# Kernel tuning notes

Hardware: AMD Instinct MI355X
Metric: run time of the kernel (lower is better)

Reference implementation:

```python
import jax, jax.numpy as jnp
import numpy as np

B, C, MID, OUT, T, N = 8, 128, 64, 128, 4, 512


def setup_inputs() -> dict:
    key = jax.random.key(0)
    ks = jax.random.split(key, 5)
    def w(k, o, i, scale):
        return (jax.random.normal(k, (o, i), jnp.float32) * scale)
    return {
        "pc": jax.random.normal(ks[0], (B, C, T, N), jnp.float32),
        "theta_w": w(ks[1], MID, C, 0.05), "theta_b": jnp.zeros((MID,), jnp.float32),
        "phi_w": w(ks[2], MID, C, 0.05), "phi_b": jnp.zeros((MID,), jnp.float32),
        "g_w": w(ks[3], MID, C, 0.05), "g_b": jnp.zeros((MID,), jnp.float32),
        "refine_w": w(ks[4], OUT, MID, 0.05), "refine_b": jnp.zeros((OUT,), jnp.float32),
    }


def reference(pc, theta_w, theta_b, phi_w, phi_b, g_w, g_b, refine_w, refine_b):
    b, c, t, n = pc.shape
    tn = t * n
    # pt_utils.Conv2d with bn=False: 1x1 conv + bias + ReLU
    def proj(wt, bs):
        h = jnp.einsum('oc,bctn->botn', wt, pc) + bs[None, :, None, None]
        return jax.nn.relu(h).reshape(b, -1, tn)  # [B, mid, TN]

    theta = proj(theta_w, theta_b).transpose(0, 2, 1)  # [B, TN, mid]
    phi = proj(phi_w, phi_b)                            # [B, mid, TN]
    g = proj(g_w, g_b).transpose(0, 2, 1)               # [B, TN, mid]

    scores = jnp.einsum('bqm,bmk->bqk', theta, phi)     # [B, TN, TN]
    corr = jax.nn.softmax(scores, axis=1)               # softmax over QUERY axis (dim=1)
    y = jnp.einsum('bqk,bkm->bmq', corr, g)             # bmm then transpose(1,2): [B, mid, TN]

    # pt_utils.Conv1d with bn=False: 1x1 conv + bias + ReLU
    refined = jax.nn.relu(jnp.einsum('om,bmq->boq', refine_w, y) + refine_b[None, :, None])
    # faithful raw reshape (row-major, same as torch) then permute, plus residual
    z = refined.reshape(b, t, n, -1).transpose(0, 3, 1, 2) + pc
    return z
```

## Files before the change

### kernel.cpp

```cpp
#include <hip/hip_runtime.h>


constexpr int NL75_TN  = 2048;
constexpr int NL75_MID = 64;
constexpr int NL75_C   = 128;
constexpr float NL75_L2E = 1.4426950408889634f;

typedef __attribute__((ext_vector_type(8))) short nl75_bf8;
typedef __attribute__((ext_vector_type(4))) float nl75_f4;

__device__ __forceinline__ unsigned short nl75_f2b(float f) {
  unsigned x = __float_as_uint(f);
  return (unsigned short)((x + 0x7fffu + ((x >> 16) & 1u)) >> 16);
}

__device__ __forceinline__ unsigned int nl75_pkbf16(float lo, float hi) {
  unsigned int r;
  asm("v_cvt_pk_bf16_f32 %0, %1, %2" : "=v"(r) : "v"(lo), "v"(hi));
  return r;
}

__device__ __forceinline__ float nl75_exp2(float x) {
  float r;
  asm("v_exp_f32 %0, %1" : "=v"(r) : "v"(x));
  return r;
}

typedef const __attribute__((address_space(1))) unsigned int* nl75_gp;
typedef __attribute__((address_space(3))) unsigned int* nl75_lp;
__device__ __forceinline__ void nl75_gld16(const void* g, void* l) {
  __builtin_amdgcn_global_load_lds((nl75_gp)g, (nl75_lp)l, 16, 0, 0);
}

__device__ __forceinline__ void nl75_stage64(const unsigned short* src,
                                             size_t pitch, unsigned short* lds,
                                             int tid) {
  const int w = tid >> 6, lane = tid & 63;
#pragma unroll
  for (int r = 0; r < 2; r++) {
    const int slot = r * 256 + w * 64 + lane;
    const int row = slot >> 3, x = slot & 7;
    const unsigned short* s =
        src + (size_t)row * pitch + ((x * 8) ^ ((row & 7) << 3));
    nl75_gld16(s, lds + (size_t)(r * 256 + w * 64) * 8);
  }
}

__global__ void NonLocalLayer_75771813036638_kernel() {}

__global__ void nl75_proj(const float* pc, const float* w0, const float* b0,
                          const float* w1, const float* b1, const float* w2,
                          const float* b2, unsigned short* thT,
                          unsigned short* phT, unsigned short* gN, int bOff,
                          int nb) {
  __shared__ float wT[NL75_C][68];
  const int bl = blockIdx.x, pj = blockIdx.y, qt = blockIdx.z;
  const int b = bOff + bl;
  const float* wp = (pj == 0) ? w0 : (pj == 1) ? w1 : w2;
  const float* bp = (pj == 0) ? b0 : (pj == 1) ? b1 : b2;
  const int tid = threadIdx.x;
  for (int i = tid; i < NL75_MID * NL75_C; i += 256)
    wT[i & 127][i >> 7] = wp[i];
  __syncthreads();
  const int qg = tid & 31, mg = tid >> 5;
  const int q = qt * 64 + qg * 2, m0 = mg * 8;
  const float* pcb = pc + (long long)b * NL75_C * NL75_TN + q;
  float acc[8][2];
#pragma unroll
  for (int i = 0; i < 8; i++) acc[i][0] = acc[i][1] = bp[m0 + i];
#pragma unroll 4
  for (int c = 0; c < NL75_C; c++) {
    const float2 p = *(const float2*)&pcb[(size_t)c * NL75_TN];
    float w8[8];
    *(float4*)&w8[0] = *(const float4*)&wT[c][m0];
    *(float4*)&w8[4] = *(const float4*)&wT[c][m0 + 4];
#pragma unroll
    for (int i = 0; i < 8; i++) {
      acc[i][0] = fmaf(w8[i], p.x, acc[i][0]);
      acc[i][1] = fmaf(w8[i], p.y, acc[i][1]);
    }
  }
  if (pj < 2) {
    unsigned int u[8];
#pragma unroll
    for (int i = 0; i < 4; i++) {
      u[i] = nl75_pkbf16(fmaxf(acc[2 * i][0], 0.0f),
                         fmaxf(acc[2 * i + 1][0], 0.0f));
      u[4 + i] = nl75_pkbf16(fmaxf(acc[2 * i][1], 0.0f),
                             fmaxf(acc[2 * i + 1][1], 0.0f));
    }
    unsigned short* dst =
        (pj == 0 ? thT : phT) + ((size_t)bl * NL75_TN + q) * 64 + m0;
    *reinterpret_cast<uint4*>(dst) = *reinterpret_cast<uint4*>(&u[0]);
    *reinterpret_cast<uint4*>(dst + 64) = *reinterpret_cast<uint4*>(&u[4]);
  } else {
    const int kin = q & 63;
    const int np = (kin >> 5) * 32 + (((kin & 15) >> 2) << 3) +
                   (((kin >> 4) & 1) << 2) + (kin & 3);
    const size_t gq = (size_t)(q & ~63) | np;
#pragma unroll
    for (int i = 0; i < 8; i++) {
      ushort2 v;
      v.x = nl75_f2b(fmaxf(acc[i][0], 0.0f));
      v.y = nl75_f2b(fmaxf(acc[i][1], 0.0f));
      *(ushort2*)&gN[((size_t)bl * NL75_MID + m0 + i) * NL75_TN + gq] = v;
    }
  }
}

__global__ void nl75_stats(const unsigned short* thT, const unsigned short* phT,
                           float* Sp, int nb, int qsplit) {
  __shared__ unsigned short thL[2][64 * 64];
  const int bl = blockIdx.x;
  const int kt = blockIdx.y & 15, qs = blockIdx.y >> 4;
  const int tid = threadIdx.x, lane = tid & 63, w = tid >> 6;
  const int l15 = lane & 15, quad = lane >> 4;
  const int k0 = kt * 128;
  const unsigned short* thB = thT + (size_t)bl * NL75_TN * 64;
  const unsigned short* phB = phT + (size_t)bl * NL75_TN * 64;
  const size_t kra = (size_t)(k0 + w * 16 + l15) * 64;
  const size_t krb = (size_t)(k0 + 64 + w * 16 + l15) * 64;
  const nl75_bf8 b0a = *(const nl75_bf8*)&phB[kra + quad * 8];
  const nl75_bf8 b1a = *(const nl75_bf8*)&phB[kra + 32 + quad * 8];
  const nl75_bf8 b0b = *(const nl75_bf8*)&phB[krb + quad * 8];
  const nl75_bf8 b1b = *(const nl75_bf8*)&phB[krb + 32 + quad * 8];
  const int qtN = 32 / qsplit, qtBeg = qs * qtN;
  nl75_stage64(thB + (size_t)(qtBeg * 64) * 64, 64, thL[0], tid);
  __syncthreads();
  float Sa = 0.0f, Sb = 0.0f;
  for (int qt = qtBeg; qt < qtBeg + qtN; qt++) {
    const int cur = (qt - qtBeg) & 1;
    if (qt + 1 < qtBeg + qtN)
      nl75_stage64(thB + (size_t)((qt + 1) * 64) * 64, 64, thL[cur ^ 1], tid);
    __builtin_amdgcn_s_setprio(1);
#pragma unroll
    for (int q16 = 0; q16 < 4; q16++) {
      const int qr = q16 * 16 + l15;
      const int sw = (qr & 7) << 3;
      const nl75_bf8 a0 = *(const nl75_bf8*)&thL[cur][qr * 64 + ((quad * 8) ^ sw)];
      const nl75_bf8 a1 =
          *(const nl75_bf8*)&thL[cur][qr * 64 + ((32 + quad * 8) ^ sw)];
      nl75_f4 ca = {0.0f, 0.0f, 0.0f, 0.0f};
      ca = __builtin_amdgcn_mfma_f32_16x16x32_bf16(a0, b0a, ca, 0, 0, 0);
      ca = __builtin_amdgcn_mfma_f32_16x16x32_bf16(a1, b1a, ca, 0, 0, 0);
      nl75_f4 cb = {0.0f, 0.0f, 0.0f, 0.0f};
      cb = __builtin_amdgcn_mfma_f32_16x16x32_bf16(a0, b0b, cb, 0, 0, 0);
      cb = __builtin_amdgcn_mfma_f32_16x16x32_bf16(a1, b1b, cb, 0, 0, 0);
      Sa += (nl75_exp2(ca[0] * NL75_L2E) + nl75_exp2(ca[1] * NL75_L2E)) +
            (nl75_exp2(ca[2] * NL75_L2E) + nl75_exp2(ca[3] * NL75_L2E));
      Sb += (nl75_exp2(cb[0] * NL75_L2E) + nl75_exp2(cb[1] * NL75_L2E)) +
            (nl75_exp2(cb[2] * NL75_L2E) + nl75_exp2(cb[3] * NL75_L2E));
    }
    __builtin_amdgcn_s_setprio(0);
    __syncthreads();
  }
  Sa += __shfl_xor(Sa, 16);
  Sa += __shfl_xor(Sa, 32);
  Sb += __shfl_xor(Sb, 16);
  Sb += __shfl_xor(Sb, 32);
  if (quad == 0) {
    const long long base = ((long long)(qs * nb + bl)) * NL75_TN + k0;
    Sp[base + w * 16 + l15] = Sa;
    Sp[base + 64 + w * 16 + l15] = Sb;
  }
}

__global__ void nl75_attn(const unsigned short* thT, const unsigned short* phT,
                          const unsigned short* gN, const float* Sp,
                          float* yPart, int nb, int ksplit, int qsplit) {
  __shared__ unsigned short phL[2][64 * 64];
  __shared__ unsigned short gL[2][64 * 64];
  __shared__ float ekL[2048];
  const int wg = blockIdx.x;
  const int bl = wg % nb;
  const int rest = wg / nb;
  const int qt = rest & 15, ks = rest >> 4;
  const int tid = threadIdx.x, lane = tid & 63, w = tid >> 6;
  const int l15 = lane & 15, quad = lane >> 4;
  const int q0 = qt * 128;
  const unsigned short* thB = thT + (size_t)bl * NL75_TN * 64;
  const unsigned short* phB = phT + (size_t)bl * NL75_TN * 64;
  const unsigned short* gB = gN + (size_t)bl * NL75_MID * NL75_TN;
  const int ktN = 32 / ksplit;
  const int ktBeg = ks * ktN, ktEnd = ktBeg + ktN;
  nl75_stage64(phB + (size_t)(ktBeg * 64) * 64, 64, phL[0], tid);
  nl75_stage64(gB + ktBeg * 64, NL75_TN, gL[0], tid);
  nl75_bf8 aq[2][2];
#pragma unroll
  for (int s = 0; s < 2; s++) {
    const size_t qr = (size_t)(q0 + s * 64 + w * 16 + l15) * 64;
    aq[s][0] = *(const nl75_bf8*)&thB[qr + quad * 8];
    aq[s][1] = *(const nl75_bf8*)&thB[qr + 32 + quad * 8];
  }
  const int kRange = ktN * 64;
  for (int kk = tid; kk < kRange; kk += 256) {
    const int k = ktBeg * 64 + kk;
    float S = 0.0f;
    for (int qs = 0; qs < qsplit; qs++)
      S += Sp[((size_t)(qs * nb + bl)) * NL75_TN + k];
    ekL[kk] = __log2f(S);
  }
  nl75_f4 yacc[2][4];
#pragma unroll
  for (int s = 0; s < 2; s++)
#pragma unroll
    for (int i = 0; i < 4; i++) yacc[s][i] = (nl75_f4){0.0f, 0.0f, 0.0f, 0.0f};
  __syncthreads();
  union Frag { nl75_bf8 h; unsigned int u[4]; };
  for (int kt = ktBeg; kt < ktEnd; kt++) {
    const int cur = (kt - ktBeg) & 1;
    if (kt + 1 < ktEnd) {
      nl75_stage64(phB + (size_t)((kt + 1) * 64) * 64, 64, phL[cur ^ 1], tid);
      nl75_stage64(gB + (kt + 1) * 64, NL75_TN, gL[cur ^ 1], tid);
    }
    const int ekBase = (kt - ktBeg) * 64;
    nl75_f4 ek[4];
#pragma unroll
    for (int t = 0; t < 4; t++)
      ek[t] = *(const nl75_f4*)&ekL[ekBase + t * 16 + quad * 4];
    __builtin_amdgcn_s_setprio(1);
    unsigned int pk[2][8];
#pragma unroll
    for (int t = 0; t < 4; t++) {
      const int krr = t * 16 + l15;
      const int sw = (krr & 7) << 3;
      const nl75_bf8 b0 =
          *(const nl75_bf8*)&phL[cur][krr * 64 + ((quad * 8) ^ sw)];
      const nl75_bf8 b1 =
          *(const nl75_bf8*)&phL[cur][krr * 64 + ((32 + quad * 8) ^ sw)];
#pragma unroll
      for (int s = 0; s < 2; s++) {
        nl75_f4 c = {0.0f, 0.0f, 0.0f, 0.0f};
        c = __builtin_amdgcn_mfma_f32_16x16x32_bf16(b0, aq[s][0], c, 0, 0, 0);
        c = __builtin_amdgcn_mfma_f32_16x16x32_bf16(b1, aq[s][1], c, 0, 0, 0);
        pk[s][t * 2 + 0] =
            nl75_pkbf16(nl75_exp2(fmaf(c[0], NL75_L2E, -ek[t][0])),
                        nl75_exp2(fmaf(c[1], NL75_L2E, -ek[t][1])));
        pk[s][t * 2 + 1] =
            nl75_pkbf16(nl75_exp2(fmaf(c[2], NL75_L2E, -ek[t][2])),
                        nl75_exp2(fmaf(c[3], NL75_L2E, -ek[t][3])));
      }
    }
#pragma unroll
    for (int mtile = 0; mtile < 4; mtile++) {
      const int m = mtile * 16 + l15;
      const int sw = (m & 7) << 3;
      const unsigned short* row = &gL[cur][m * 64];
      Frag bg0, bg1;
      bg0.h = *(const nl75_bf8*)&row[(quad * 8) ^ sw];
      bg1.h = *(const nl75_bf8*)&row[(32 + quad * 8) ^ sw];
#pragma unroll
      for (int s = 0; s < 2; s++) {
        Frag a0, a1;
        a0.u[0] = pk[s][0]; a0.u[1] = pk[s][1];
        a0.u[2] = pk[s][2]; a0.u[3] = pk[s][3];
        a1.u[0] = pk[s][4]; a1.u[1] = pk[s][5];
        a1.u[2] = pk[s][6]; a1.u[3] = pk[s][7];
        yacc[s][mtile] = __builtin_amdgcn_mfma_f32_16x16x32_bf16(
            a0.h, bg0.h, yacc[s][mtile], 0, 0, 0);
        yacc[s][mtile] = __builtin_amdgcn_mfma_f32_16x16x32_bf16(
            a1.h, bg1.h, yacc[s][mtile], 0, 0, 0);
      }
    }
    __builtin_amdgcn_s_setprio(0);
    __syncthreads();
  }
  float* yB = yPart + ((size_t)(ks * nb + bl) * NL75_MID) * NL75_TN;
#pragma unroll
  for (int s = 0; s < 2; s++)
#pragma unroll
    for (int mtile = 0; mtile < 4; mtile++) {
      float4 v = make_float4(yacc[s][mtile][0], yacc[s][mtile][1],
                             yacc[s][mtile][2], yacc[s][mtile][3]);
      *(float4*)&yB[(size_t)(mtile * 16 + l15) * NL75_TN + q0 + s * 64 +
                    w * 16 + quad * 4] = v;
    }
}

__global__ void nl75_yred(const float* yPart, float* y, int nb, int ksplit) {
  const size_t tot = (size_t)nb * NL75_MID * NL75_TN / 4;
  const size_t stride = tot;
  const float4* src = (const float4*)yPart;
  float4* dst = (float4*)y;
  for (size_t i = (size_t)blockIdx.x * 256 + threadIdx.x; i < tot;
       i += (size_t)gridDim.x * 256) {
    float4 a = src[i];
    for (int ks = 1; ks < ksplit; ks++) {
      float4 b = src[(size_t)ks * stride + i];
      a.x += b.x; a.y += b.y; a.z += b.z; a.w += b.w;
    }
    dst[i] = a;
  }
}

__global__ void nl75_refsc(const float* yIn, const float* rW, const float* rB,
                           const float* pc, float* outP, int bOff, int nb,
                           int ksplit) {
  __shared__ float rwS[32][66];
  __shared__ float yS[NL75_MID][132];
  const int bl = blockIdx.x, cg = blockIdx.y, t = blockIdx.z;
  const int b = bOff + bl, c0 = cg * 8, tid = threadIdx.x;
  for (int i = tid; i < 32 * NL75_MID; i += 256) {
    int oh = i >> 6, m = i & 63;
    rwS[oh][m] = rW[(long long)(t * 32 + oh) * NL75_MID + m];
  }
  if (ksplit == 1) {
    const float* yB0 = yIn + (size_t)bl * NL75_MID * NL75_TN;
    for (int i = tid; i < NL75_MID * 32; i += 256) {
      int m = i >> 5, r = i & 31;
      int i16 = r >> 1, half = r & 1;
      const float4 v = *(const float4*)&yB0[(size_t)m * NL75_TN + i16 * 128 +
                                            c0 + half * 4];
      *(float4*)&yS[m][i16 * 8 + half * 4] = v;
    }
  } else {
    for (int i = tid; i < NL75_MID * 128; i += 256) {
      int m = i >> 7, qi = i & 127;
      int i16 = qi >> 3, cl = qi & 7;
      long long off = (long long)m * NL75_TN + i16 * 128 + c0 + cl;
      float v = 0.0f;
      for (int ks = 0; ks < ksplit; ks++)
        v += yIn[((long long)(ks * nb + bl) * NL75_MID) * NL75_TN + off];
      yS[m][qi] = v;
    }
  }
  __syncthreads();
  const int oh0 = (tid >> 5) * 4;
  const int q4 = (tid & 31) * 4;
  float acc[4][4];
#pragma unroll
  for (int i = 0; i < 4; i++) {
    float bias = rB[t * 32 + oh0 + i];
#pragma unroll
    for (int j = 0; j < 4; j++) acc[i][j] = bias;
  }
  for (int m = 0; m < NL75_MID; m++) {
    float yv[4];
#pragma unroll
    for (int j = 0; j < 4; j++) yv[j] = yS[m][q4 + j];
#pragma unroll
    for (int i = 0; i < 4; i++) {
      float w = rwS[oh0 + i][m];
#pragma unroll
      for (int j = 0; j < 4; j++) acc[i][j] = fmaf(w, yv[j], acc[i][j]);
    }
  }
  __syncthreads();
  float* outS = &yS[0][0];
  const int NP = 516;
#pragma unroll
  for (int i = 0; i < 4; i++) {
    const int oh = oh0 + i;
#pragma unroll
    for (int j = 0; j < 4; j++) {
      const int qi = q4 + j;
      outS[(qi & 7) * NP + oh * 16 + (qi >> 3)] = fmaxf(acc[i][j], 0.0f);
    }
  }
  __syncthreads();
  const size_t obase = (((size_t)b * 128 + c0) * 4 + t) * 512;
#pragma unroll
  for (int ii = 0; ii < 4; ii++) {
    const int fi = ii * 256 + tid;
    const int cl = fi >> 7, n0 = (fi & 127) * 4;
    float4 v = *(const float4*)&outS[cl * NP + n0];
    const size_t gi = obase + (size_t)cl * 4 * 512 + n0;
    const float4 p = *(const float4*)&pc[gi];
    v.x += p.x; v.y += p.y; v.z += p.z; v.w += p.w;
    *(float4*)&outP[gi] = v;
  }
}

extern "C" void kernel_launch(void* const* d_in, const int* in_sizes, int n_in,
                              void* d_out, int out_size, void* d_ws, size_t ws_size,
                              hipStream_t stream) {
  const float* pc = (const float*)d_in[0];
  const float* tw = (const float*)d_in[1];
  const float* tb = (const float*)d_in[2];
  const float* pw = (const float*)d_in[3];
  const float* pb = (const float*)d_in[4];
  const float* gw = (const float*)d_in[5];
  const float* gb = (const float*)d_in[6];
  const float* rw = (const float*)d_in[7];
  const float* rb = (const float*)d_in[8];
  float* out = (float*)d_out;

  const size_t yPB = (size_t)NL75_MID * NL75_TN;
  auto need = [&](int nb, int qs, int ks) -> size_t {
    return (3ull * nb * NL75_TN * 64 * 2) +
           ((size_t)qs * nb * NL75_TN + ((size_t)ks * nb + nb) * yPB) * 4;
  };

  int nb, qsplit, ksplit;
  if (ws_size >= need(8, 8, 8))      { nb = 8; qsplit = 8; ksplit = 8; }
  else if (ws_size >= need(8, 1, 1)) { nb = 8; qsplit = 1; ksplit = 1; }
  else                               { nb = 1; qsplit = 1; ksplit = 1; }
  const int nloop = 8 / nb;

  unsigned short* thT = (unsigned short*)d_ws;
  unsigned short* phT = thT + (size_t)nb * NL75_TN * 64;
  unsigned short* gN = phT + (size_t)nb * NL75_TN * 64;
  float* Sp = (float*)(gN + (size_t)nb * NL75_MID * NL75_TN);
  float* yPart = Sp + (size_t)qsplit * nb * NL75_TN;
  float* yFull = (ksplit > 1) ? yPart + (size_t)ksplit * nb * yPB : yPart;

  for (int l = 0; l < nloop; l++) {
    const int bOff = l * nb;
    nl75_proj<<<dim3(nb, 3, 32), 256, 0, stream>>>(pc, tw, tb, pw, pb, gw, gb,
                                                   thT, phT, gN, bOff, nb);
    nl75_stats<<<dim3(nb, 16 * qsplit), 256, 0, stream>>>(thT, phT, Sp, nb,
                                                          qsplit);
    nl75_attn<<<dim3(16 * ksplit * nb), 256, 0, stream>>>(
        thT, phT, gN, Sp, yPart, nb, ksplit, qsplit);
    if (ksplit > 1) {
      nl75_yred<<<dim3(1024), 256, 0, stream>>>(yPart, yFull, nb, ksplit);
      nl75_refsc<<<dim3(nb, 16, 4), 256, 0, stream>>>(yFull, rw, rb, pc, out,
                                                      bOff, nb, 1);
    } else {
      nl75_refsc<<<dim3(nb, 16, 4), 256, 0, stream>>>(yPart, rw, rb, pc, out,
                                                      bOff, nb, 1);
    }
  }
}
```

Baseline: 139.3 us.

## Split attention query tile across 8 waves instead of 4 with 2 subtiles

The attention kernel now launches 512 threads per block. Each of the 8 waves handles one 16-query subtile instead of two, and the stage helper issues one 16-byte global-to-LDS load per thread. This roughly halves per-wave registers (accumulators, packed probabilities, query fragments) and raises wave-level parallelism to hide exp and MFMA latency. The cost is that phi/g LDS fragments are now read by twice as many waves, and every block still pays the same sync overhead.

```diff
diff --git a/kernel.cpp b/kernel.cpp
--- a/kernel.cpp
+++ b/kernel.cpp
@@ -44,6 +44,16 @@
         src + (size_t)row * pitch + ((x * 8) ^ ((row & 7) << 3));
     nl75_gld16(s, lds + (size_t)(r * 256 + w * 64) * 8);
   }
+}
+
+__device__ __forceinline__ void nl75_stage64w(const unsigned short* src,
+                                              size_t pitch,
+                                              unsigned short* lds, int tid) {
+  const int w = tid >> 6;
+  const int row = tid >> 3, x = tid & 7;
+  const unsigned short* s =
+      src + (size_t)row * pitch + ((x * 8) ^ ((row & 7) << 3));
+  nl75_gld16(s, lds + (size_t)(w * 64) * 8);
 }
 
 __global__ void NonLocalLayer_75771813036638_kernel() {}
@@ -165,6 +175,7 @@
   }
 }
 
+__launch_bounds__(512, 8)
 __global__ void nl75_attn(const unsigned short* thT, const unsigned short* phT,
                           const unsigned short* gN, const float* Sp,
                           float* yPart, int nb, int ksplit, int qsplit) {
@@ -183,43 +194,36 @@
   const unsigned short* gB = gN + (size_t)bl * NL75_MID * NL75_TN;
   const int ktN = 32 / ksplit;
   const int ktBeg = ks * ktN, ktEnd = ktBeg + ktN;
-  nl75_stage64(phB + (size_t)(ktBeg * 64) * 64, 64, phL[0], tid);
-  nl75_stage64(gB + ktBeg * 64, NL75_TN, gL[0], tid);
-  nl75_bf8 aq[2][2];
-#pragma unroll
-  for (int s = 0; s < 2; s++) {
-    const size_t qr = (size_t)(q0 + s * 64 + w * 16 + l15) * 64;
-    aq[s][0] = *(const nl75_bf8*)&thB[qr + quad * 8];
-    aq[s][1] = *(const nl75_bf8*)&thB[qr + 32 + quad * 8];
+  nl75_stage64w(phB + (size_t)(ktBeg * 64) * 64, 64, phL[0], tid);
+  nl75_stage64w(gB + ktBeg * 64, NL75_TN, gL[0], tid);
+  nl75_bf8 aq0, aq1;
+  {
+    const size_t qr = (size_t)(q0 + w * 16 + l15) * 64;
+    aq0 = *(const nl75_bf8*)&thB[qr + quad * 8];
+    aq1 = *(const nl75_bf8*)&thB[qr + 32 + quad * 8];
   }
   const int kRange = ktN * 64;
-  for (int kk = tid; kk < kRange; kk += 256) {
+  for (int kk = tid; kk < kRange; kk += 512) {
     const int k = ktBeg * 64 + kk;
     float S = 0.0f;
     for (int qs = 0; qs < qsplit; qs++)
       S += Sp[((size_t)(qs * nb + bl)) * NL75_TN + k];
     ekL[kk] = __log2f(S);
   }
-  nl75_f4 yacc[2][4];
-#pragma unroll
-  for (int s = 0; s < 2; s++)
-#pragma unroll
-    for (int i = 0; i < 4; i++) yacc[s][i] = (nl75_f4){0.0f, 0.0f, 0.0f, 0.0f};
+  nl75_f4 yacc[4];
+#pragma unroll
+  for (int i = 0; i < 4; i++) yacc[i] = (nl75_f4){0.0f, 0.0f, 0.0f, 0.0f};
   __syncthreads();
   union Frag { nl75_bf8 h; unsigned int u[4]; };
   for (int kt = ktBeg; kt < ktEnd; kt++) {
     const int cur = (kt - ktBeg) & 1;
     if (kt + 1 < ktEnd) {
-      nl75_stage64(phB + (size_t)((kt + 1) * 64) * 64, 64, phL[cur ^ 1], tid);
-      nl75_stage64(gB + (kt + 1) * 64, NL75_TN, gL[cur ^ 1], tid);
+      nl75_stage64w(phB + (size_t)((kt + 1) * 64) * 64, 64, phL[cur ^ 1], tid);
+      nl75_stage64w(gB + (kt + 1) * 64, NL75_TN, gL[cur ^ 1], tid);
     }
     const int ekBase = (kt - ktBeg) * 64;
-    nl75_f4 ek[4];
-#pragma unroll
-    for (int t = 0; t < 4; t++)
-      ek[t] = *(const nl75_f4*)&ekL[ekBase + t * 16 + quad * 4];
     __builtin_amdgcn_s_setprio(1);
-    unsigned int pk[2][8];
+    unsigned int pk[8];
 #pragma unroll
     for (int t = 0; t < 4; t++) {
       const int krr = t * 16 + l15;
@@ -228,19 +232,18 @@
           *(const nl75_bf8*)&phL[cur][krr * 64 + ((quad * 8) ^ sw)];
       const nl75_bf8 b1 =
           *(const nl75_bf8*)&phL[cur][krr * 64 + ((32 + quad * 8) ^ sw)];
-#pragma unroll
-      for (int s = 0; s < 2; s++) {
-        nl75_f4 c = {0.0f, 0.0f, 0.0f, 0.0f};
-        c = __builtin_amdgcn_mfma_f32_16x16x32_bf16(b0, aq[s][0], c, 0, 0, 0);
-        c = __builtin_amdgcn_mfma_f32_16x16x32_bf16(b1, aq[s][1], c, 0, 0, 0);
-        pk[s][t * 2 + 0] =
-            nl75_pkbf16(nl75_exp2(fmaf(c[0], NL75_L2E, -ek[t][0])),
-                        nl75_exp2(fmaf(c[1], NL75_L2E, -ek[t][1])));
-        pk[s][t * 2 + 1] =
-            nl75_pkbf16(nl75_exp2(fmaf(c[2], NL75_L2E, -ek[t][2])),
-                        nl75_exp2(fmaf(c[3], NL75_L2E, -ek[t][3])));
-      }
-    }
+      const nl75_f4 ek = *(const nl75_f4*)&ekL[ekBase + t * 16 + quad * 4];
+      nl75_f4 c = {0.0f, 0.0f, 0.0f, 0.0f};
+      c = __builtin_amdgcn_mfma_f32_16x16x32_bf16(b0, aq0, c, 0, 0, 0);
+      c = __builtin_amdgcn_mfma_f32_16x16x32_bf16(b1, aq1, c, 0, 0, 0);
+      pk[t * 2 + 0] = nl75_pkbf16(nl75_exp2(fmaf(c[0], NL75_L2E, -ek[0])),
+                                  nl75_exp2(fmaf(c[1], NL75_L2E, -ek[1])));
+      pk[t * 2 + 1] = nl75_pkbf16(nl75_exp2(fmaf(c[2], NL75_L2E, -ek[2])),
+                                  nl75_exp2(fmaf(c[3], NL75_L2E, -ek[3])));
+    }
+    Frag a0, a1;
+    a0.u[0] = pk[0]; a0.u[1] = pk[1]; a0.u[2] = pk[2]; a0.u[3] = pk[3];
+    a1.u[0] = pk[4]; a1.u[1] = pk[5]; a1.u[2] = pk[6]; a1.u[3] = pk[7];
 #pragma unroll
     for (int mtile = 0; mtile < 4; mtile++) {
       const int m = mtile * 16 + l15;
@@ -249,32 +252,22 @@
       Frag bg0, bg1;
       bg0.h = *(const nl75_bf8*)&row[(quad * 8) ^ sw];
       bg1.h = *(const nl75_bf8*)&row[(32 + quad * 8) ^ sw];
-#pragma unroll
-      for (int s = 0; s < 2; s++) {
-        Frag a0, a1;
-        a0.u[0] = pk[s][0]; a0.u[1] = pk[s][1];
-        a0.u[2] = pk[s][2]; a0.u[3] = pk[s][3];
-        a1.u[0] = pk[s][4]; a1.u[1] = pk[s][5];
-        a1.u[2] = pk[s][6]; a1.u[3] = pk[s][7];
-        yacc[s][mtile] = __builtin_amdgcn_mfma_f32_16x16x32_bf16(
-            a0.h, bg0.h, yacc[s][mtile], 0, 0, 0);
-        yacc[s][mtile] = __builtin_amdgcn_mfma_f32_16x16x32_bf16(
-            a1.h, bg1.h, yacc[s][mtile], 0, 0, 0);
-      }
+      yacc[mtile] = __builtin_amdgcn_mfma_f32_16x16x32_bf16(a0.h, bg0.h,
+                                                            yacc[mtile], 0, 0, 0);
+      yacc[mtile] = __builtin_amdgcn_mfma_f32_16x16x32_bf16(a1.h, bg1.h,
+                                                            yacc[mtile], 0, 0, 0);
     }
     __builtin_amdgcn_s_setprio(0);
     __syncthreads();
   }
   float* yB = yPart + ((size_t)(ks * nb + bl) * NL75_MID) * NL75_TN;
 #pragma unroll
-  for (int s = 0; s < 2; s++)
-#pragma unroll
-    for (int mtile = 0; mtile < 4; mtile++) {
-      float4 v = make_float4(yacc[s][mtile][0], yacc[s][mtile][1],
-                             yacc[s][mtile][2], yacc[s][mtile][3]);
-      *(float4*)&yB[(size_t)(mtile * 16 + l15) * NL75_TN + q0 + s * 64 +
-                    w * 16 + quad * 4] = v;
-    }
+  for (int mtile = 0; mtile < 4; mtile++) {
+    float4 v = make_float4(yacc[mtile][0], yacc[mtile][1], yacc[mtile][2],
+                           yacc[mtile][3]);
+    *(float4*)&yB[(size_t)(mtile * 16 + l15) * NL75_TN + q0 + w * 16 +
+                  quad * 4] = v;
+  }
 }
 
 __global__ void nl75_yred(const float* yPart, float* y, int nb, int ksplit) {
@@ -410,7 +403,7 @@
                                                    thT, phT, gN, bOff, nb);
     nl75_stats<<<dim3(nb, 16 * qsplit), 256, 0, stream>>>(thT, phT, Sp, nb,
                                                           qsplit);
-    nl75_attn<<<dim3(16 * ksplit * nb), 256, 0, stream>>>(
+    nl75_attn<<<dim3(16 * ksplit * nb), 512, 0, stream>>>(
         thT, phT, gN, Sp, yPart, nb, ksplit, qsplit);
     if (ksplit > 1) {
       nl75_yred<<<dim3(1024), 256, 0, stream>>>(yPart, yFull, nb, ksplit);
```

Measured after the change: 136.8 us, median of 2. Within noise of the previous version (-1.8%).
